# Performance work log

Measured on AMD Instinct MI355X. Metric: run time of the kernel, lower is better.

Reference implementation:

```python
import jax, jax.numpy as jnp
import numpy as np

N_HEAD = 8


def setup_inputs() -> dict:
    key = jax.random.key(0)
    ks = jax.random.split(key, 12)
    b, l, d_q, d_o, h, w = 32, 64, 1024, 512, 32, 32

    def rn(k, shape, s=0.02):
        return jax.random.normal(k, shape, jnp.float32) * s

    return {
        "q": jax.random.normal(ks[0], (b, l, d_q), jnp.float32),
        "v": jax.random.normal(ks[1], (b, d_o, h, w), jnp.float32),
        "mask": jax.random.bernoulli(ks[2], 0.2, (b, l)),
        "w_qs_w": rn(ks[3], (d_o, d_q)), "w_qs_b": jnp.zeros((d_o,), jnp.float32),
        "w_qs_att_w": rn(ks[4], (1, d_o)), "w_qs_att_b": jnp.zeros((1,), jnp.float32),
        "w_kc_w": rn(ks[5], (d_o, d_o, 1, 1)), "w_kc_b": jnp.zeros((d_o,), jnp.float32),
        "w_kd_w": rn(ks[6], (d_o, d_o, 1, 1)), "w_kd_b": jnp.zeros((d_o,), jnp.float32),
        "w_vs_w": rn(ks[7], (d_o, d_o, 1, 1)), "w_vs_b": jnp.zeros((d_o,), jnp.float32),
        "w_m_w": rn(ks[8], (1, d_o, 3, 3)), "w_m_b": jnp.zeros((1,), jnp.float32),
        "bn_gamma": jnp.ones((d_o,), jnp.float32), "bn_beta": jnp.zeros((d_o,), jnp.float32),
        "bn_mean": jnp.zeros((d_o,), jnp.float32), "bn_var": jnp.ones((d_o,), jnp.float32),
    }


def _conv1x1(x, wgt, bias):  # x: (b,c,h,w), wgt: (o,c,1,1)
    return jnp.einsum('bchw,oc->bohw', x, wgt[:, :, 0, 0]) + bias[None, :, None, None]


def reference(q, v, mask, w_qs_w, w_qs_b, w_qs_att_w, w_qs_att_b,
              w_kc_w, w_kc_b, w_kd_w, w_kd_b, w_vs_w, w_vs_b,
              w_m_w, w_m_b, bn_gamma, bn_beta, bn_mean, bn_var):
    b, l, _ = q.shape
    _, c, h, w_ = v.shape
    n = N_HEAD
    dk = c // n
    temp = float(np.power(dk, 0.5))  # sqrt(d_o // n_head)
    residual = v

    qp = q @ w_qs_w.T + w_qs_b                       # (b,l,d_o)
    flap = qp @ w_qs_att_w.T + w_qs_att_b            # (b,l,1)
    flap = jnp.where(mask[:, :, None], -1e9, flap)
    flap = jax.nn.softmax(flap, axis=-1)             # softmax over size-1 dim -> all ones (faithful to torch)

    kc = _conv1x1(v, w_kc_w, w_kc_b).reshape(b, n, dk, h * w_).transpose(0, 1, 3, 2)  # (b,n,hw,dk)
    kd = _conv1x1(v, w_kd_w, w_kd_b).reshape(b, n, dk, h * w_).transpose(0, 1, 3, 2)
    vh = _conv1x1(v, w_vs_w, w_vs_b).reshape(b, n, dk, h * w_).transpose(0, 1, 3, 2)
    qh = qp.reshape(b, l, n, dk).transpose(0, 2, 1, 3)                                 # (b,n,l,dk)

    # Collect: bmm -> weight by flap -> reduce over l -> softmax over hw -> bmm with v
    attn_col = jnp.einsum('bnld,bnsd->bnls', qh, kc)                 # (b,n,l,hw)
    attn_col = (attn_col * flap[:, None, :, :]).sum(axis=2, keepdims=True) / temp  # (b,n,1,hw)
    attn_col = jax.nn.softmax(attn_col, axis=-1)
    attn = jnp.einsum('bnus,bnsd->bnud', attn_col, vh)               # (b,n,1,dk)

    # Diffuse: bmm -> weight by flap^T -> reduce over l -> sigmoid -> outer product
    attn_dif = jnp.einsum('bnsd,bnld->bnsl', kd, qh)                 # (b,n,hw,l)
    flap_t = flap.transpose(0, 2, 1)[:, None]                        # (b,1,1,l)
    attn_dif = jax.nn.sigmoid((attn_dif * flap_t).sum(-1, keepdims=True) / temp)  # (b,n,hw,1)
    output = attn_dif * attn                                         # (b,n,hw,dk)

    # Faithful to torch permute(0,1,4,3,2).view(b,-1,h,w) (requires h==w)
    out = output.reshape(b, n, h, w_, dk).transpose(0, 1, 4, 3, 2).reshape(b, c, h, w_)
    attn_map = out

    m = jax.lax.conv_general_dilated(out, w_m_w, (1, 1), 'SAME',
                                     dimension_numbers=('NCHW', 'OIHW', 'NCHW'))
    m_attn = (m + w_m_b[None, :, None, None]).reshape(b, h * w_)

    eps = 1e-5  # BatchNorm2d eval mode
    scale = bn_gamma / jnp.sqrt(bn_var + eps)
    out = (out - bn_mean[None, :, None, None]) * scale[None, :, None, None] + bn_beta[None, :, None, None]
    out = out + residual
    out = jnp.where(out >= 0, out, 0.1 * out)  # LeakyReLU(0.1)
    return (out, m_attn, attn_map)
```

## Files before the change

kernel.cpp:

```cpp
#include <hip/hip_runtime.h>


#define BB 32
#define LL 64
#define DQn 1024
#define CCn 512
#define NH 8
#define DKn 64
#define HWn 1024

typedef unsigned short u16;
typedef unsigned int u32;

__device__ __forceinline__ float bfr(u16 u) {
    return __uint_as_float(((u32)u) << 16);
}
__device__ __forceinline__ u16 f2bf(float f) {
    u32 x = __float_as_uint(f);
    u32 r = (x + 0x7FFFu + ((x >> 16) & 1u)) >> 16;
    return (u16)r;
}

__global__ void k1_qsum_pre(const float* __restrict__ q, float* __restrict__ qsp) {
    int b = blockIdx.y;
    int dq = blockIdx.x * 256 + threadIdx.x;
    const float* qp = q + (size_t)b * LL * DQn + dq;
    float acc = 0.f;
#pragma unroll 8
    for (int l = 0; l < LL; ++l) acc += qp[l * DQn];
    qsp[b * DQn + dq] = acc;
}

__global__ void k2_qsum(const float* __restrict__ qsp, const float* __restrict__ w,
                        const float* __restrict__ bias, float* __restrict__ qs) {
    int dof = blockIdx.x;
    int t = threadIdx.x;
    int b = t & 31, ch = t >> 5;
    const float* wrow = w + (size_t)dof * DQn + ch * 128;
    const float* qrow = qsp + (size_t)b * DQn + ch * 128;
    float acc = 0.f;
#pragma unroll 8
    for (int i = 0; i < 128; i += 4) {
        float4 wv = *reinterpret_cast<const float4*>(wrow + i);
        float4 qv = *reinterpret_cast<const float4*>(qrow + i);
        acc += wv.x * qv.x + wv.y * qv.y + wv.z * qv.z + wv.w * qv.w;
    }
    __shared__ float scr[256];
    scr[t] = acc;
    __syncthreads();
    if (t < 32) {
        float a = 0.f;
#pragma unroll
        for (int c2 = 0; c2 < 8; ++c2) a += scr[c2 * 32 + t];
        qs[t * CCn + dof] = a + 64.f * bias[dof];
    }
}

__global__ void k3_wq(const float* __restrict__ qs,
                      const float* __restrict__ wkc, const float* __restrict__ bkc,
                      const float* __restrict__ wkd, const float* __restrict__ bkd,
                      float* __restrict__ wq, float* __restrict__ bq) {
    int cc = blockIdx.x, wsel = blockIdx.y, b = blockIdx.z;
    const float* w = wsel ? wkd : wkc;
    int cl = threadIdx.x & 31, n = threadIdx.x >> 5;
    int c = cc * 32 + cl;
    const float* qrow = qs + b * CCn + n * DKn;
    const float* wrow = w + (size_t)(n * DKn) * CCn + c;
    float acc = 0.f;
#pragma unroll 8
    for (int d = 0; d < DKn; ++d)
        acc += qrow[d] * wrow[(size_t)d * CCn];
    wq[((size_t)b * CCn + c) * 16 + wsel * 8 + n] = acc;
    if (cc == 0 && b == 0) {
        const float* bw = wsel ? bkd : bkc;
        int pp = threadIdx.x, bb = pp >> 3, nn = pp & 7;
        float a2 = 0.f;
#pragma unroll 8
        for (int d = 0; d < DKn; ++d)
            a2 += qs[bb * CCn + nn * DKn + d] * bw[nn * DKn + d];
        bq[wsel * 256 + pp] = a2;
    }
}

__global__ void __launch_bounds__(256) k46_scorepv(
        const float* __restrict__ v, const float* __restrict__ wq,
        const float* __restrict__ bq, float* __restrict__ dsig,
        float* __restrict__ pvp, float* __restrict__ sums) {
    int sc = blockIdx.x, b = blockIdx.y;
    __shared__ u16 vt[CCn * 33];
    __shared__ float red[4][32][17];
    __shared__ float et[32 * 8];
    int t = threadIdx.x;
    int s0 = sc * 32;

    {
        int s = t & 31, c2 = t >> 5;
        const float* vb = v + ((size_t)(b * CCn + c2 * 64) << 10) + s0 + s;
#pragma unroll 8
        for (int cr = 0; cr < 64; ++cr)
            vt[(c2 * 64 + cr) * 33 + s] = f2bf(vb[(size_t)cr << 10]);
    }
    __syncthreads();

    {
        int s = t & 31, g = t >> 5;
        float ak[16];
#pragma unroll
        for (int j = 0; j < 16; ++j) ak[j] = 0.f;
        const float* wqb = wq + ((size_t)b * CCn + g * 64) * 16;
#pragma unroll 4
        for (int i = 0; i < 64; ++i) {
            float vv = bfr(vt[(g * 64 + i) * 33 + s]);
            const float* wc = wqb + i * 16;
#pragma unroll
            for (int j = 0; j < 16; ++j) ak[j] += wc[j] * vv;
        }
#pragma unroll
        for (int j = 0; j < 16; ++j) ak[j] += __shfl_xor(ak[j], 32);
        int wv = t >> 6;
        if ((t & 63) < 32) {
#pragma unroll
            for (int j = 0; j < 16; ++j) red[wv][s][j] = ak[j];
        }
    }
    __syncthreads();
    if (t < 32) {
        int s = t;
#pragma unroll
        for (int n = 0; n < NH; ++n) {
            float rc = red[0][s][n] + red[1][s][n] + red[2][s][n] + red[3][s][n];
            float rd = red[0][s][8 + n] + red[1][s][8 + n] + red[2][s][8 + n] + red[3][s][8 + n];
            float skc = (rc + bq[b * 8 + n]) * 0.125f;
            float skd = (rd + bq[256 + b * 8 + n]) * 0.125f;
            et[s * 8 + n] = __expf(skc);
            dsig[(b * NH + n) * HWn + s0 + s] = 1.f / (1.f + __expf(-skd));
        }
    }
    __syncthreads();
    if (t < 8) {
        float a = 0.f;
#pragma unroll
        for (int s = 0; s < 32; ++s) a += et[s * 8 + t];
        sums[(b * NH + t) * 32 + sc] = a;
    }
    {
        float acc0[NH], acc1[NH];
#pragma unroll
        for (int n = 0; n < NH; ++n) { acc0[n] = 0.f; acc1[n] = 0.f; }
#pragma unroll 2
        for (int s = 0; s < 32; ++s) {
            float4 ea = *reinterpret_cast<const float4*>(et + s * 8);
            float4 eb = *reinterpret_cast<const float4*>(et + s * 8 + 4);
            float va = bfr(vt[t * 33 + s]);
            float vb2 = bfr(vt[(t + 256) * 33 + s]);
            acc0[0] += ea.x * va; acc0[1] += ea.y * va; acc0[2] += ea.z * va; acc0[3] += ea.w * va;
            acc0[4] += eb.x * va; acc0[5] += eb.y * va; acc0[6] += eb.z * va; acc0[7] += eb.w * va;
            acc1[0] += ea.x * vb2; acc1[1] += ea.y * vb2; acc1[2] += ea.z * vb2; acc1[3] += ea.w * vb2;
            acc1[4] += eb.x * vb2; acc1[5] += eb.y * vb2; acc1[6] += eb.z * vb2; acc1[7] += eb.w * vb2;
        }
        size_t base = ((size_t)sc * BB + b) * NH;
#pragma unroll
        for (int n = 0; n < NH; ++n) {
            pvp[(base + n) * CCn + t] = acc0[n];
            pvp[(base + n) * CCn + t + 256] = acc1[n];
        }
    }
}

__global__ void k7_attn(const float* __restrict__ pvp, const float* __restrict__ sums,
                        const float* __restrict__ wvs, const float* __restrict__ bvs,
                        float* __restrict__ attn) {
    int n = blockIdx.x, b = blockIdx.y;
    __shared__ float pvl[CCn];
    __shared__ float scr[64 * 5];
    __shared__ float sinv;
    int t = threadIdx.x;
    if (t == 0) {
        float a = 0.f;
#pragma unroll
        for (int sc = 0; sc < 32; ++sc) a += sums[(b * NH + n) * 32 + sc];
        sinv = 1.f / a;
    }
    for (int c = t; c < CCn; c += 256) {
        float acc = 0.f;
#pragma unroll 4
        for (int sc = 0; sc < 32; ++sc)
            acc += pvp[(((size_t)sc * BB + b) * NH + n) * CCn + c];
        pvl[c] = acc;
    }
    __syncthreads();
    int d = t & 63, qq = t >> 6;
    const float* wrow = wvs + (size_t)(n * DKn + d) * CCn + qq * 128;
    const float* pq = pvl + qq * 128;
    float acc = 0.f;
#pragma unroll 4
    for (int i = 0; i < 128; ++i) acc += pq[i] * wrow[i];
    scr[d * 5 + qq] = acc;
    __syncthreads();
    if (t < 64) {
        float a = (scr[t * 5] + scr[t * 5 + 1] + scr[t * 5 + 2] + scr[t * 5 + 3]) * sinv
                + bvs[n * DKn + t];
        attn[(b * NH + n) * DKn + t] = a;
    }
}

__global__ void k8_mattn(const float* __restrict__ dsig, const float* __restrict__ attn,
                         const float* __restrict__ wm, const float* __restrict__ wmb,
                         float* __restrict__ out1) {
    int b = blockIdx.x;
    __shared__ float dst[NH * 1056];
    __shared__ float al[CCn];
    __shared__ float A2[NH * 9];
    int t = threadIdx.x;
    al[t] = attn[b * CCn + t];
    al[t + 256] = attn[b * CCn + t + 256];
    for (int g = t; g < NH * HWn; g += 256) {
        int n = g >> 10, s = g & 1023;
        dst[n * 1056 + (s & 31) * 33 + (s >> 5)] = dsig[b * NH * HWn + g];
    }
    __syncthreads();
    if (t < 72) {
        int n = t / 9, tap = t % 9;
        float acc = 0.f;
#pragma unroll 8
        for (int d = 0; d < DKn; ++d)
            acc += al[n * DKn + d] * wm[(n * DKn + d) * 9 + tap];
        A2[t] = acc;
    }
    __syncthreads();
    float bm = wmb[0];
    for (int pos = t; pos < HWn; pos += 256) {
        int y = pos >> 5, x = pos & 31;
        float m = 0.f;
#pragma unroll
        for (int n = 0; n < NH; ++n) {
            const float* dn = dst + n * 1056;
#pragma unroll
            for (int dy = 0; dy < 3; ++dy) {
                int yy = y + dy - 1;
                if ((unsigned)yy < 32u) {
#pragma unroll
                    for (int dx = 0; dx < 3; ++dx) {
                        int xx = x + dx - 1;
                        if ((unsigned)xx < 32u)
                            m += A2[n * 9 + dy * 3 + dx] * dn[yy * 33 + xx];
                    }
                }
            }
        }
        out1[b * HWn + pos] = m + bm;
    }
}

__global__ void __launch_bounds__(256) k9_out(
        const float* __restrict__ v, const float* __restrict__ dsig,
        const float* __restrict__ attn,
        const float* __restrict__ gamma, const float* __restrict__ beta,
        const float* __restrict__ mean, const float* __restrict__ var,
        float* __restrict__ out0, float* __restrict__ out2) {
    int dh = blockIdx.x, n = blockIdx.y, b = blockIdx.z;
    __shared__ float dst[1056];
    __shared__ float al[16], bnA[16], bnB[16];
    int t = threadIdx.x;
#pragma unroll
    for (int k = 0; k < 4; ++k) {
        int s = t + k * 256;
        dst[(s & 31) * 33 + (s >> 5)] = dsig[(b * NH + n) * HWn + s];
    }
    if (t < 16) {
        int d = dh * 16 + t;
        al[t] = attn[(b * NH + n) * DKn + d];
        int ch = n * DKn + d;
        float A = gamma[ch] * rsqrtf(var[ch] + 1e-5f);
        bnA[t] = A;
        bnB[t] = beta[ch] - mean[ch] * A;
    }
    __syncthreads();
    int y = t >> 3, x = (t & 7) * 4;
    const float* dr = dst + y * 33 + x;
#pragma unroll 2
    for (int k = 0; k < 16; ++k) {
        int d = dh * 16 + k;
        size_t base = (((size_t)(b * CCn + n * DKn + d)) << 10) + y * 32 + x;
        float4 v4 = *reinterpret_cast<const float4*>(v + base);
        float a = al[k], A = bnA[k], Bc = bnB[k];
        float p0 = a * dr[0], p1 = a * dr[1], p2 = a * dr[2], p3 = a * dr[3];
        float4 mo = make_float4(p0, p1, p2, p3);
        *reinterpret_cast<float4*>(out2 + base) = mo;
        float o0 = p0 * A + Bc + v4.x;
        float o1 = p1 * A + Bc + v4.y;
        float o2 = p2 * A + Bc + v4.z;
        float o3 = p3 * A + Bc + v4.w;
        o0 = o0 < 0.f ? 0.1f * o0 : o0;
        o1 = o1 < 0.f ? 0.1f * o1 : o1;
        o2 = o2 < 0.f ? 0.1f * o2 : o2;
        o3 = o3 < 0.f ? 0.1f * o3 : o3;
        float4 oo = make_float4(o0, o1, o2, o3);
        *reinterpret_cast<float4*>(out0 + base) = oo;
    }
}

extern "C" void kernel_launch(void* const* d_in, const int* in_sizes, int n_in,
                              void* d_out, int out_size, void* d_ws, size_t ws_size,
                              hipStream_t stream) {
    (void)in_sizes; (void)n_in; (void)out_size; (void)ws_size;
    const float* q   = (const float*)d_in[0];
    const float* v   = (const float*)d_in[1];
    const float* wqs = (const float*)d_in[3];
    const float* bqs = (const float*)d_in[4];
    const float* wkc = (const float*)d_in[7];
    const float* bkc = (const float*)d_in[8];
    const float* wkd = (const float*)d_in[9];
    const float* bkd = (const float*)d_in[10];
    const float* wvs = (const float*)d_in[11];
    const float* bvs = (const float*)d_in[12];
    const float* wm  = (const float*)d_in[13];
    const float* wmb = (const float*)d_in[14];
    const float* gam = (const float*)d_in[15];
    const float* bet = (const float*)d_in[16];
    const float* mea = (const float*)d_in[17];
    const float* var = (const float*)d_in[18];

    float* ws = (float*)d_ws;
    float* qsp  = ws + 0;
    float* qs   = ws + 32768;
    float* wq   = ws + 49152;
    float* bq   = ws + 311296;
    float* dsig = ws + 311808;
    float* sums = ws + 573952;
    float* attn = ws + 582144;
    float* pvp  = ws + 598528;

    float* out0 = (float*)d_out;
    float* out1 = out0 + 16777216;
    float* out2 = out1 + 32768;

    k1_qsum_pre<<<dim3(4, 32), 256, 0, stream>>>(q, qsp);
    k2_qsum<<<dim3(512), 256, 0, stream>>>(qsp, wqs, bqs, qs);
    k3_wq<<<dim3(16, 2, 32), 256, 0, stream>>>(qs, wkc, bkc, wkd, bkd, wq, bq);
    k46_scorepv<<<dim3(32, 32), 256, 0, stream>>>(v, wq, bq, dsig, pvp, sums);
    k7_attn<<<dim3(8, 32), 256, 0, stream>>>(pvp, sums, wvs, bvs, attn);
    k8_mattn<<<dim3(32), 256, 0, stream>>>(dsig, attn, wm, wmb, out1);
    k9_out<<<dim3(4, 8, 32), 256, 0, stream>>>(v, dsig, attn, gam, bet, mea, var, out0, out2);
}
```

Before: 346.7 us.

## Fuse pipeline into persistent megakernel with grid barriers and resident bf16 v tile

```diff
diff --git a/kernel.cpp b/kernel.cpp
--- a/kernel.cpp
+++ b/kernel.cpp
@@ -8,6 +8,7 @@
 #define NH 8
 #define DKn 64
 #define HWn 1024
+#define NBLK 512
 
 typedef unsigned short u16;
 typedef unsigned int u32;
@@ -20,6 +21,322 @@
     u32 r = (x + 0x7FFFu + ((x >> 16) & 1u)) >> 16;
     return (u16)r;
 }
+
+#define POOLB 78080
+
+struct MArgs {
+    const float *q, *v, *wqs, *bqs, *wkc, *bkc, *wkd, *bkd, *wvs, *bvs, *wm, *wmb,
+                *gam, *bet, *mea, *var;
+    float *qsp, *qs, *wq, *bq, *dsig, *sums, *attn, *A2g, *pvp;
+    u32* bar;
+    float *out0, *out1, *out2;
+};
+
+__device__ __forceinline__ void gbar(u32* bar, int i) {
+    __syncthreads();
+    if (threadIdx.x == 0) {
+        __threadfence();
+        u32 old = atomicAdd(&bar[i], 1u);
+        if (old == (u32)(NBLK - 1)) {
+            atomicExch(&bar[8 + i], 1u);
+        } else {
+            int it = 0;
+            while (atomicAdd(&bar[8 + i], 0u) == 0u) {
+                __builtin_amdgcn_s_sleep(2);
+                if (++it > (1 << 18)) break;
+            }
+        }
+        __threadfence();
+    }
+    __syncthreads();
+}
+
+__global__ void kinit(u32* bar) {
+    if (threadIdx.x < 16) bar[threadIdx.x] = 0u;
+}
+
+#define PVACC(accv, eA, eB, vf) \
+    accv[0] += eA.x * (vf); accv[1] += eA.y * (vf); accv[2] += eA.z * (vf); accv[3] += eA.w * (vf); \
+    accv[4] += eB.x * (vf); accv[5] += eB.y * (vf); accv[6] += eB.z * (vf); accv[7] += eB.w * (vf);
+
+__global__ void __launch_bounds__(256, 2) mega(MArgs A) {
+    extern __shared__ char pool[];
+    u32*   vtd = (u32*)pool;
+    float* red = (float*)(pool + 65536);
+    float* etb = (float*)(pool + 69888);
+    float* ext = (float*)(pool + 71936);
+    float* scr2  = red;
+    float* pvl   = etb;
+    float* scr7  = red;
+    float* al7   = red + 320;
+    float* sinvp = red + 384;
+    float* dsl   = red;
+    float* A2l   = red + 512;
+    u16*   k8s   = (u16*)etb;
+    float* al    = ext;
+    float* bnA   = ext + 512;
+    float* bnB   = ext + 1024;
+
+    int t = threadIdx.x;
+    int bid = blockIdx.x;
+    int sc = bid & 15, b = bid >> 4;
+    int s0 = sc * 64;
+
+    if (bid < 128) {
+        int b1 = bid >> 2;
+        int dq = (bid & 3) * 256 + t;
+        const float* qp = A.q + (size_t)b1 * LL * DQn + dq;
+        float acc = 0.f;
+#pragma unroll 8
+        for (int l = 0; l < LL; ++l) acc += qp[l * DQn];
+        A.qsp[b1 * DQn + dq] = acc;
+    }
+
+    {
+        int sp = t & 31, c2 = t >> 5;
+        const float* vb = A.v + (((size_t)(b * CCn + c2 * 64)) << 10) + s0 + sp * 2;
+#pragma unroll 8
+        for (int cr = 0; cr < 64; ++cr) {
+            int r = c2 * 64 + cr;
+            float2 xv = *reinterpret_cast<const float2*>(vb + ((size_t)cr << 10));
+            u32 w = (u32)f2bf(xv.x) | ((u32)f2bf(xv.y) << 16);
+            vtd[r * 32 + (sp ^ (r & 31))] = w;
+        }
+    }
+    gbar(A.bar, 0);
+
+    {
+        int dof = bid;
+        int b2 = t & 31, ch = t >> 5;
+        const float* wrow = A.wqs + (size_t)dof * DQn + ch * 128;
+        const float* qrow = A.qsp + (size_t)b2 * DQn + ch * 128;
+        float acc = 0.f;
+#pragma unroll 8
+        for (int i = 0; i < 128; i += 4) {
+            float4 wv = *reinterpret_cast<const float4*>(wrow + i);
+            float4 qv = *reinterpret_cast<const float4*>(qrow + i);
+            acc += wv.x * qv.x + wv.y * qv.y + wv.z * qv.z + wv.w * qv.w;
+        }
+        scr2[t] = acc;
+        __syncthreads();
+        if (t < 32) {
+            float a = 0.f;
+#pragma unroll
+            for (int c2 = 0; c2 < 8; ++c2) a += scr2[c2 * 32 + t];
+            A.qs[t * CCn + dof] = a + 64.f * A.bqs[dof];
+        }
+    }
+    gbar(A.bar, 1);
+
+    {
+        int cl = t & 31, n3 = t >> 5;
+        int c = sc * 32 + cl;
+#pragma unroll
+        for (int wsel = 0; wsel < 2; ++wsel) {
+            const float* w = wsel ? A.wkd : A.wkc;
+            const float* qrow = A.qs + b * CCn + n3 * DKn;
+            const float* wrow = w + (size_t)(n3 * DKn) * CCn + c;
+            float acc = 0.f;
+#pragma unroll 8
+            for (int d = 0; d < DKn; ++d) acc += qrow[d] * wrow[(size_t)d * CCn];
+            A.wq[((size_t)b * CCn + c) * 16 + wsel * 8 + n3] = acc;
+            if (bid == 0) {
+                const float* bw = wsel ? A.bkd : A.bkc;
+                int bb = t >> 3, nn = t & 7;
+                float a2 = 0.f;
+#pragma unroll 8
+                for (int d = 0; d < DKn; ++d)
+                    a2 += A.qs[bb * CCn + nn * DKn + d] * bw[nn * DKn + d];
+                A.bq[wsel * 256 + t] = a2;
+            }
+        }
+    }
+    for (int i = t; i < 64 * 17; i += 256) red[i] = 0.f;
+    gbar(A.bar, 2);
+
+    {
+        int s = t & 63, g = t >> 6;
+        int sp = s >> 1, sh = (s & 1) << 4;
+        float ak[16];
+#pragma unroll
+        for (int j = 0; j < 16; ++j) ak[j] = 0.f;
+        const float* wqb = A.wq + ((size_t)b * CCn + g * 128) * 16;
+#pragma unroll 4
+        for (int i = 0; i < 128; ++i) {
+            int r = g * 128 + i;
+            u32 wv = vtd[r * 32 + (sp ^ (r & 31))];
+            float vvf = bfr((u16)(wv >> sh));
+            const float* wc = wqb + i * 16;
+#pragma unroll
+            for (int j = 0; j < 16; ++j) ak[j] += wc[j] * vvf;
+        }
+#pragma unroll
+        for (int j = 0; j < 16; ++j) atomicAdd(&red[s * 17 + j], ak[j]);
+    }
+    __syncthreads();
+    if (t < 64) {
+        int s = t;
+#pragma unroll
+        for (int n = 0; n < NH; ++n) {
+            float rc = red[s * 17 + n];
+            float rd = red[s * 17 + 8 + n];
+            float skc = (rc + A.bq[b * 8 + n]) * 0.125f;
+            float skd = (rd + A.bq[256 + b * 8 + n]) * 0.125f;
+            etb[s * 8 + n] = __expf(skc);
+            A.dsig[((size_t)(b * NH + n)) * HWn + s0 + s] = 1.f / (1.f + __expf(-skd));
+        }
+    }
+    __syncthreads();
+    if (t < 8) {
+        float a = 0.f;
+#pragma unroll
+        for (int s = 0; s < 64; ++s) a += etb[s * 8 + t];
+        A.sums[(b * NH + t) * 16 + sc] = a;
+    }
+    {
+        float acc0[NH], acc1[NH];
+#pragma unroll
+        for (int n = 0; n < NH; ++n) { acc0[n] = 0.f; acc1[n] = 0.f; }
+        int c0 = t, c1 = t + 256;
+        int m = t & 31;
+#pragma unroll 2
+        for (int sp = 0; sp < 32; ++sp) {
+            u32 w0 = vtd[c0 * 32 + (sp ^ m)];
+            u32 w1 = vtd[c1 * 32 + (sp ^ m)];
+            float va0 = bfr((u16)(w0 & 0xffffu)), va1 = bfr((u16)(w0 >> 16));
+            float vb0 = bfr((u16)(w1 & 0xffffu)), vb1 = bfr((u16)(w1 >> 16));
+            float4 e0a = *reinterpret_cast<const float4*>(etb + sp * 16);
+            float4 e0b = *reinterpret_cast<const float4*>(etb + sp * 16 + 4);
+            float4 e1a = *reinterpret_cast<const float4*>(etb + sp * 16 + 8);
+            float4 e1b = *reinterpret_cast<const float4*>(etb + sp * 16 + 12);
+            PVACC(acc0, e0a, e0b, va0)
+            PVACC(acc0, e1a, e1b, va1)
+            PVACC(acc1, e0a, e0b, vb0)
+            PVACC(acc1, e1a, e1b, vb1)
+        }
+        size_t base = ((size_t)sc * BB + b) * NH;
+#pragma unroll
+        for (int n = 0; n < NH; ++n) {
+            A.pvp[(base + n) * CCn + c0] = acc0[n];
+            A.pvp[(base + n) * CCn + c1] = acc1[n];
+        }
+    }
+    gbar(A.bar, 3);
+
+    if (bid < 256) {
+        int n = bid & 7, b7 = bid >> 3;
+        for (int c = t; c < CCn; c += 256) {
+            float acc = 0.f;
+#pragma unroll 4
+            for (int s2 = 0; s2 < 16; ++s2)
+                acc += A.pvp[(((size_t)s2 * BB + b7) * NH + n) * CCn + c];
+            pvl[c] = acc;
+        }
+        if (t == 0) {
+            float a = 0.f;
+#pragma unroll
+            for (int s2 = 0; s2 < 16; ++s2) a += A.sums[(b7 * NH + n) * 16 + s2];
+            sinvp[0] = 1.f / a;
+        }
+        __syncthreads();
+        {
+            int d = t & 63, qq = t >> 6;
+            const float* wrow = A.wvs + (size_t)(n * DKn + d) * CCn + qq * 128;
+            const float* pq = pvl + qq * 128;
+            float acc = 0.f;
+#pragma unroll 4
+            for (int i = 0; i < 128; ++i) acc += pq[i] * wrow[i];
+            scr7[d * 5 + qq] = acc;
+        }
+        __syncthreads();
+        if (t < 64) {
+            float a = (scr7[t * 5] + scr7[t * 5 + 1] + scr7[t * 5 + 2] + scr7[t * 5 + 3])
+                      * sinvp[0] + A.bvs[n * DKn + t];
+            A.attn[(b7 * NH + n) * DKn + t] = a;
+            al7[t] = a;
+        }
+        __syncthreads();
+        if (t < 9) {
+            float acc = 0.f;
+#pragma unroll 8
+            for (int d2 = 0; d2 < DKn; ++d2)
+                acc += al7[d2] * A.wm[(n * DKn + d2) * 9 + t];
+            A.A2g[b7 * 72 + n * 9 + t] = acc;
+        }
+    }
+    gbar(A.bar, 4);
+
+    int y0 = sc * 2;
+    {
+        for (int idx = t; idx < CCn; idx += 256) {
+            al[idx] = A.attn[b * CCn + idx];
+            float Av = A.gam[idx] * rsqrtf(A.var[idx] + 1e-5f);
+            bnA[idx] = Av;
+            bnB[idx] = A.bet[idx] - A.mea[idx] * Av;
+        }
+        for (int idx = t; idx < NH * 64; idx += 256) {
+            int n = idx >> 6, r6 = idx & 63;
+            int yb2 = r6 >> 5, x = r6 & 31;
+            dsl[idx] = A.dsig[((size_t)(b * NH + n)) * HWn + x * 32 + y0 + yb2];
+        }
+        for (int idx = t; idx < 4 * NH * 32; idx += 256) {
+            int ry = idx >> 8, n = (idx >> 5) & 7, x = idx & 31;
+            int ycol = y0 - 1 + ry;
+            float dvv = 0.f;
+            if ((unsigned)ycol < 32u)
+                dvv = A.dsig[((size_t)(b * NH + n)) * HWn + x * 32 + ycol];
+            k8s[idx] = f2bf(dvv);
+        }
+        if (t < 72) A2l[t] = A.A2g[b * 72 + t];
+    }
+    __syncthreads();
+    {
+        int l = t & 63, wv = t >> 6;
+        int csub = l >> 4, yb = (l >> 3) & 1, x0 = (l & 7) * 4;
+        int sl = yb * 32 + x0;
+#pragma unroll 2
+        for (int it = 0; it < 32; ++it) {
+            int c = it * 16 + wv * 4 + csub;
+            int n = c >> 6;
+            int m = c & 31;
+            u32 w0 = vtd[c * 32 + ((sl >> 1) ^ m)];
+            u32 w1 = vtd[c * 32 + (((sl >> 1) + 1) ^ m)];
+            float4 dv = *reinterpret_cast<const float4*>(dsl + n * 64 + sl);
+            float a = al[c], Ac = bnA[c], Bc = bnB[c];
+            float p0 = a * dv.x, p1 = a * dv.y, p2 = a * dv.z, p3 = a * dv.w;
+            size_t ob = (((size_t)(b * CCn + c)) << 10) + (u32)((y0 + yb) * 32 + x0);
+            *reinterpret_cast<float4*>(A.out2 + ob) = make_float4(p0, p1, p2, p3);
+            float o0 = fmaf(p0, Ac, Bc) + bfr((u16)(w0 & 0xffffu));
+            float o1 = fmaf(p1, Ac, Bc) + bfr((u16)(w0 >> 16));
+            float o2 = fmaf(p2, Ac, Bc) + bfr((u16)(w1 & 0xffffu));
+            float o3 = fmaf(p3, Ac, Bc) + bfr((u16)(w1 >> 16));
+            o0 = o0 < 0.f ? 0.1f * o0 : o0;
+            o1 = o1 < 0.f ? 0.1f * o1 : o1;
+            o2 = o2 < 0.f ? 0.1f * o2 : o2;
+            o3 = o3 < 0.f ? 0.1f * o3 : o3;
+            *reinterpret_cast<float4*>(A.out0 + ob) = make_float4(o0, o1, o2, o3);
+        }
+    }
+    if (t < 64) {
+        int y = y0 + (t >> 5), x = t & 31;
+        float msum = 0.f;
+#pragma unroll
+        for (int n = 0; n < NH; ++n) {
+#pragma unroll
+            for (int dy = 0; dy < 3; ++dy) {
+                int ry = (t >> 5) + dy;
+#pragma unroll
+                for (int dx = 0; dx < 3; ++dx) {
+                    int xx = x + dx - 1;
+                    if ((unsigned)xx < 32u)
+                        msum += A2l[n * 9 + dy * 3 + dx] * bfr(k8s[ry * 256 + n * 32 + xx]);
+                }
+            }
+        }
+        A.out1[b * HWn + y * 32 + x] = msum + A.wmb[0];
+    }
+}
+
 
 __global__ void k1_qsum_pre(const float* __restrict__ q, float* __restrict__ qsp) {
     int b = blockIdx.y;
@@ -92,7 +409,6 @@
     __shared__ float et[32 * 8];
     int t = threadIdx.x;
     int s0 = sc * 32;
-
     {
         int s = t & 31, c2 = t >> 5;
         const float* vb = v + ((size_t)(b * CCn + c2 * 64) << 10) + s0 + s;
@@ -101,7 +417,6 @@
             vt[(c2 * 64 + cr) * 33 + s] = f2bf(vb[(size_t)cr << 10]);
     }
     __syncthreads();
-
     {
         int s = t & 31, g = t >> 5;
         float ak[16];
@@ -322,6 +637,39 @@
     const float* var = (const float*)d_in[18];
 
     float* ws = (float*)d_ws;
+    float* out0 = (float*)d_out;
+    float* out1 = out0 + 16777216;
+    float* out2 = out1 + 32768;
+
+    static int mode = -1;
+    if (mode < 0) {
+        hipError_t e = hipFuncSetAttribute(reinterpret_cast<const void*>(mega),
+                                           hipFuncAttributeMaxDynamicSharedMemorySize,
+                                           POOLB);
+        mode = (e == hipSuccess) ? 1 : 0;
+    }
+
+    if (mode == 1) {
+        MArgs a;
+        a.q = q; a.v = v; a.wqs = wqs; a.bqs = bqs; a.wkc = wkc; a.bkc = bkc;
+        a.wkd = wkd; a.bkd = bkd; a.wvs = wvs; a.bvs = bvs; a.wm = wm; a.wmb = wmb;
+        a.gam = gam; a.bet = bet; a.mea = mea; a.var = var;
+        a.qsp  = ws;
+        a.qs   = ws + 32768;
+        a.wq   = ws + 49152;
+        a.bq   = ws + 311296;
+        a.dsig = ws + 311808;
+        a.sums = ws + 573952;
+        a.attn = ws + 578048;
+        a.A2g  = ws + 594432;
+        a.pvp  = ws + 596736;
+        a.bar  = (u32*)(ws + 2693888);
+        a.out0 = out0; a.out1 = out1; a.out2 = out2;
+        kinit<<<dim3(1), dim3(64), 0, stream>>>(a.bar);
+        mega<<<dim3(NBLK), dim3(256), POOLB, stream>>>(a);
+        return;
+    }
+
     float* qsp  = ws + 0;
     float* qs   = ws + 32768;
     float* wq   = ws + 49152;
@@ -331,10 +679,6 @@
     float* attn = ws + 582144;
     float* pvp  = ws + 598528;
 
-    float* out0 = (float*)d_out;
-    float* out1 = out0 + 16777216;
-    float* out2 = out1 + 32768;
-
     k1_qsum_pre<<<dim3(4, 32), 256, 0, stream>>>(q, qsp);
     k2_qsum<<<dim3(512), 256, 0, stream>>>(qsp, wqs, bqs, qs);
     k3_wq<<<dim3(16, 2, 32), 256, 0, stream>>>(qs, wkc, bkc, wkd, bkd, wq, bq);
```

Measured after the change: 553.8 us. +59.7%, slower.
